# Kernel tuning notes

Hardware: AMD Instinct MI355X
Metric: run time of the kernel (lower is better)

The kernel has to match this reference:

```python
import jax, jax.numpy as jnp
import numpy as np

N_NODES = 100000


def _gcn_layer(x, src, dst, W, b, n_nodes):
    # x: [N, Cin]; src/dst already include self-loops
    h = x @ W  # [N, Cout]
    deg = jax.ops.segment_sum(jnp.ones_like(dst, dtype=h.dtype), dst,
                              num_segments=n_nodes)  # in-degree incl. self-loop
    dinv = jnp.where(deg > 0, deg ** -0.5, 0.0)
    norm = dinv[src] * dinv[dst]  # [E]
    msg = h[src] * norm[:, None]  # [E, Cout]
    out = jax.ops.segment_sum(msg, dst, num_segments=n_nodes)
    return out + b


def setup_inputs() -> dict:
    key = jax.random.key(0)
    k1, k2, k3, k4, k5, k6, k7 = jax.random.split(key, 7)
    E = 6400000
    x = jax.random.normal(k1, (N_NODES, 5), dtype=jnp.float32)
    edge_index = jax.random.randint(k2, (2, E), 0, N_NODES, dtype=jnp.int64)
    edge_f = jax.random.normal(k3, (E,), dtype=jnp.float32)
    edge_attr = jax.random.normal(k4, (E, 1), dtype=jnp.float32)
    # GCNConv params (glorot-ish scale)
    W1 = jax.random.normal(k5, (5, 8), dtype=jnp.float32) * (1.0 / np.sqrt(5))
    b1 = jnp.zeros((8,), dtype=jnp.float32)
    W2 = jax.random.normal(k6, (8, 5), dtype=jnp.float32) * (1.0 / np.sqrt(8))
    b2 = jnp.zeros((5,), dtype=jnp.float32)
    return {"x": x, "edge_index": edge_index, "edge_f": edge_f,
            "edge_attr": edge_attr, "W1": W1, "b1": b1, "W2": W2, "b2": b2}


def reference(x, edge_index, edge_f, edge_attr, W1, b1, W2, b2):
    n = x.shape[0]
    loops = jnp.arange(n, dtype=edge_index.dtype)
    src = jnp.concatenate([edge_index[0], loops])  # add self-loops (PyG default)
    dst = jnp.concatenate([edge_index[1], loops])
    h = _gcn_layer(x, src, dst, W1, b1, n)
    h = _gcn_layer(h, src, dst, W2, b2, n)
    return h
```

## Files before the change

kernel.cpp:

```cpp
#include <hip/hip_runtime.h>


#define TPB 256
#define VPB 256
#define B_BITS 8
#define MAXB 512
#define CAP 17408
#define NBLK_E 512
#define EPB 12500
#define SCT 512
#define DGT 512

typedef int int4e __attribute__((ext_vector_type(4)));
__device__ __forceinline__ int4e ntload4(const int* p) {
    return __builtin_nontemporal_load((const int4e*)p);
}
__device__ __forceinline__ int ntload(const int* p) {
    return __builtin_nontemporal_load(p);
}

__global__ void k_init(int B, int* __restrict__ bpos) {
    int b = blockIdx.x * blockDim.x + threadIdx.x;
    if (b < B) bpos[b] = b * CAP;
}

__global__ __launch_bounds__(SCT) void k_scat(const int* __restrict__ src,
        const int* __restrict__ dst, int E, int B,
        int* __restrict__ bpos, int* __restrict__ pairs) {
    __shared__ int sorted[EPB];
    __shared__ int hist[MAXB], scn[MAXB], cur[MAXB], gbase[MAXB];
    int t = threadIdx.x;
    for (int i = t; i < MAXB; i += SCT) hist[i] = 0;
    __syncthreads();
    int lo = blockIdx.x * EPB;
    int n = min(E - lo, EPB);
    int n4 = n & ~3;
    for (int i = t * 4; i < n4; i += SCT * 4) {
        int4e d4 = ntload4(dst + lo + i);
        atomicAdd(&hist[d4.x >> B_BITS], 1);
        atomicAdd(&hist[d4.y >> B_BITS], 1);
        atomicAdd(&hist[d4.z >> B_BITS], 1);
        atomicAdd(&hist[d4.w >> B_BITS], 1);
    }
    for (int i = n4 + t; i < n; i += SCT)
        atomicAdd(&hist[dst[lo + i] >> B_BITS], 1);
    __syncthreads();
    if (t < MAXB) scn[t] = hist[t];
    __syncthreads();
    for (int off = 1; off < MAXB; off <<= 1) {
        int v = (t >= off && t < MAXB) ? scn[t - off] : 0;
        __syncthreads();
        if (t < MAXB) scn[t] += v;
        __syncthreads();
    }
    if (t < MAXB) {
        int h = hist[t];
        cur[t] = scn[t] - h;
        gbase[t] = (t < B && h) ? atomicAdd(&bpos[t], h) : 0;
    }
    __syncthreads();
    for (int i = t * 4; i < n4; i += SCT * 4) {
        int4e d4 = ntload4(dst + lo + i);
        int4e s4 = ntload4(src + lo + i);
        int p;
        p = atomicAdd(&cur[d4.x >> B_BITS], 1); sorted[p] = (s4.x << B_BITS) | (d4.x & (VPB - 1));
        p = atomicAdd(&cur[d4.y >> B_BITS], 1); sorted[p] = (s4.y << B_BITS) | (d4.y & (VPB - 1));
        p = atomicAdd(&cur[d4.z >> B_BITS], 1); sorted[p] = (s4.z << B_BITS) | (d4.z & (VPB - 1));
        p = atomicAdd(&cur[d4.w >> B_BITS], 1); sorted[p] = (s4.w << B_BITS) | (d4.w & (VPB - 1));
    }
    for (int i = n4 + t; i < n; i += SCT) {
        int d = dst[lo + i], s = src[lo + i];
        int p = atomicAdd(&cur[d >> B_BITS], 1);
        sorted[p] = (s << B_BITS) | (d & (VPB - 1));
    }
    __syncthreads();
    int wave = t >> 6, lane = t & 63;
    for (int b2 = wave; b2 < B; b2 += (SCT >> 6)) {
        int h = hist[b2];
        int st = scn[b2] - h;
        int gb = gbase[b2];
        for (int j = lane; j < h; j += 64)
            pairs[gb + j] = sorted[st + j];
    }
}

__global__ __launch_bounds__(DGT) void k_degxs(const int* __restrict__ pairs,
        const int* __restrict__ bpos, int N,
        const float* __restrict__ x,
        unsigned int* __restrict__ jinfo, float* __restrict__ xs) {
    __shared__ int hist[VPB];
    __shared__ int scn[VPB];
    int t = threadIdx.x, b = blockIdx.x;
    if (t < VPB) hist[t] = 0;
    __syncthreads();
    int base = b * CAP;
    int n = bpos[b] - base, n4 = n & ~3;
    for (int i = t * 4; i < n4; i += DGT * 4) {
        int4e p = ntload4(pairs + base + i);
        atomicAdd(&hist[p.x & (VPB - 1)], 1);
        atomicAdd(&hist[p.y & (VPB - 1)], 1);
        atomicAdd(&hist[p.z & (VPB - 1)], 1);
        atomicAdd(&hist[p.w & (VPB - 1)], 1);
    }
    for (int i = n4 + t; i < n; i += DGT)
        atomicAdd(&hist[pairs[base + i] & (VPB - 1)], 1);
    __syncthreads();
    if (t < VPB) scn[t] = hist[t];
    __syncthreads();
    for (int off = 1; off < VPB; off <<= 1) {
        int v = (t >= off && t < VPB) ? scn[t - off] : 0;
        __syncthreads();
        if (t < VPB) scn[t] += v;
        __syncthreads();
    }
    int node = b * VPB + t;
    if (t < VPB && node < N) {
        int h = hist[t];
        int start = base + scn[t] - h;
        jinfo[node] = ((unsigned int)start << 9) | (unsigned int)h;
        float di = rsqrtf((float)(h + 1));
        const float* xp = x + (size_t)node * 5;
        float4 v4 = make_float4(xp[0] * di, xp[1] * di, xp[2] * di, xp[3] * di);
        *(float4*)(xs + (size_t)node * 8) = v4;
        xs[(size_t)node * 8 + 4] = xp[4] * di;
    }
}

__global__ __launch_bounds__(1024) void k_agg1(const int* __restrict__ pairs_,
        const int* __restrict__ bpos, const unsigned int* __restrict__ jinfo,
        const float* __restrict__ xs, const float* __restrict__ b1,
        const float* __restrict__ W1, const float* __restrict__ W2,
        float* __restrict__ h2s, int N) {
    __shared__ int csr[CAP];
    __shared__ int js[VPB], ct[VPB], cur[VPB];
    int* pairs = (int*)pairs_;
    int t = threadIdx.x, b = blockIdx.x;
    int base = b * CAP;
    if (t < VPB) {
        int node = b * VPB + t;
        int s = 0, c = 0;
        if (node < N) {
            unsigned int u = jinfo[node];
            s = (int)(u >> 9) - base;
            c = (int)(u & 511u);
        }
        js[t] = s; ct[t] = c; cur[t] = s;
    }
    __syncthreads();
    int n = bpos[b] - base, n4 = n & ~3;
    for (int i = t * 4; i < n4; i += 1024 * 4) {
        int4e p = ntload4(pairs + base + i);
        int q;
        q = atomicAdd(&cur[p.x & (VPB - 1)], 1); csr[q] = p.x >> B_BITS;
        q = atomicAdd(&cur[p.y & (VPB - 1)], 1); csr[q] = p.y >> B_BITS;
        q = atomicAdd(&cur[p.z & (VPB - 1)], 1); csr[q] = p.z >> B_BITS;
        q = atomicAdd(&cur[p.w & (VPB - 1)], 1); csr[q] = p.w >> B_BITS;
    }
    for (int i = n4 + t; i < n; i += 1024) {
        int p = pairs[base + i];
        int q = atomicAdd(&cur[p & (VPB - 1)], 1);
        csr[q] = p >> B_BITS;
    }
    __syncthreads();
    for (int i = t; i < n; i += 1024)
        __builtin_nontemporal_store(csr[i], pairs + base + i);
    int lane = t & 3, ln = t >> 2;
    int node = b * VPB + ln;
    if (node >= N) return;
    int s0 = js[ln], cn = ct[ln];
    float a0 = 0.f, a1 = 0.f, a2 = 0.f, a3 = 0.f, a4 = 0.f;
    int j = lane;
    for (; j + 4 < cn; j += 8) {
        int sA = csr[s0 + j];
        int sB = csr[s0 + j + 4];
        const float* pA = xs + (size_t)sA * 8;
        const float* pB = xs + (size_t)sB * 8;
        float4 xA = *(const float4*)pA; float eA = pA[4];
        float4 xB = *(const float4*)pB; float eB = pB[4];
        a0 += xA.x + xB.x; a1 += xA.y + xB.y; a2 += xA.z + xB.z;
        a3 += xA.w + xB.w; a4 += eA + eB;
    }
    if (j < cn) {
        int sA = csr[s0 + j];
        const float* pA = xs + (size_t)sA * 8;
        float4 xA = *(const float4*)pA;
        a0 += xA.x; a1 += xA.y; a2 += xA.z; a3 += xA.w; a4 += pA[4];
    }
#pragma unroll
    for (int d = 1; d < 4; d <<= 1) {
        a0 += __shfl_xor(a0, d); a1 += __shfl_xor(a1, d);
        a2 += __shfl_xor(a2, d); a3 += __shfl_xor(a3, d);
        a4 += __shfl_xor(a4, d);
    }
    const float* sp = xs + (size_t)node * 8;
    float4 sx = *(const float4*)sp;
    float tc[5];
    tc[0] = a0 + sx.x; tc[1] = a1 + sx.y; tc[2] = a2 + sx.z;
    tc[3] = a3 + sx.w; tc[4] = a4 + sp[4];
    float di = rsqrtf((float)(cn + 1));
    float o1[8];
#pragma unroll
    for (int jj = 0; jj < 8; ++jj) {
        float h = 0.f;
#pragma unroll
        for (int c = 0; c < 5; ++c) h += tc[c] * W1[c * 8 + jj];
        o1[jj] = h * di + b1[jj];
    }
    {
        float h = 0.f;
#pragma unroll
        for (int jj = 0; jj < 8; ++jj) h += o1[jj] * W2[jj * 5 + lane];
        h2s[(size_t)node * 8 + lane] = h * di;
        if (lane == 0) {
            float h4 = 0.f;
#pragma unroll
            for (int jj = 0; jj < 8; ++jj) h4 += o1[jj] * W2[jj * 5 + 4];
            h2s[(size_t)node * 8 + 4] = h4 * di;
        }
    }
}

__global__ __launch_bounds__(TPB) void k_agg2(const int* __restrict__ pairs,
        const unsigned int* __restrict__ jinfo, const float* __restrict__ h2s,
        const float* __restrict__ b2, float* __restrict__ out, int N) {
    int gid = blockIdx.x * blockDim.x + threadIdx.x;
    int node = gid >> 3, lane = gid & 7;
    if (node >= N) return;
    unsigned int u = jinfo[node];
    int jsa = (int)(u >> 9), cn = (int)(u & 511u);
    float a0 = 0.f, a1 = 0.f, a2 = 0.f, a3 = 0.f, a4 = 0.f;
    int j = lane;
    for (; j + 8 < cn; j += 16) {
        int sA = ntload(pairs + jsa + j);
        int sB = ntload(pairs + jsa + j + 8);
        const float* pA = h2s + (size_t)sA * 8;
        const float* pB = h2s + (size_t)sB * 8;
        float4 xA = *(const float4*)pA; float eA = pA[4];
        float4 xB = *(const float4*)pB; float eB = pB[4];
        a0 += xA.x + xB.x; a1 += xA.y + xB.y; a2 += xA.z + xB.z;
        a3 += xA.w + xB.w; a4 += eA + eB;
    }
    if (j < cn) {
        int sA = ntload(pairs + jsa + j);
        const float* pA = h2s + (size_t)sA * 8;
        float4 xA = *(const float4*)pA;
        a0 += xA.x; a1 += xA.y; a2 += xA.z; a3 += xA.w; a4 += pA[4];
    }
#pragma unroll
    for (int d = 1; d < 8; d <<= 1) {
        a0 += __shfl_xor(a0, d); a1 += __shfl_xor(a1, d);
        a2 += __shfl_xor(a2, d); a3 += __shfl_xor(a3, d);
        a4 += __shfl_xor(a4, d);
    }
    if (lane == 0) {
        float di = rsqrtf((float)(cn + 1));
        const float* sr = h2s + (size_t)node * 8;
        float* op = out + (size_t)node * 5;
        op[0] = (a0 + sr[0]) * di + b2[0];
        op[1] = (a1 + sr[1]) * di + b2[1];
        op[2] = (a2 + sr[2]) * di + b2[2];
        op[3] = (a3 + sr[3]) * di + b2[3];
        op[4] = (a4 + sr[4]) * di + b2[4];
    }
}

extern "C" void kernel_launch(void* const* d_in, const int* in_sizes, int n_in,
                              void* d_out, int out_size, void* d_ws, size_t ws_size,
                              hipStream_t stream) {
    const float* x   = (const float*)d_in[0];
    const int*  eidx = (const int*)d_in[1];
    const float* b1 = (const float*)d_in[5];
    const float* W1 = (const float*)d_in[4];
    const float* W2 = (const float*)d_in[6];
    const float* b2 = (const float*)d_in[7];
    float* out = (float*)d_out;

    const int N = in_sizes[0] / 5;
    const int E = in_sizes[1] / 2;
    const int* src = eidx;
    const int* dst = eidx + E;

    const int B = (N + VPB - 1) / VPB;

    int*   pairs = (int*)d_ws;
    float* xs    = (float*)(pairs + (size_t)B * CAP);
    float* h2s   = xs + (size_t)8 * N;
    unsigned int* jinfo = (unsigned int*)(h2s + (size_t)8 * N);
    int*   bpos  = (int*)(jinfo + N);

    const int g8N = (8 * N + TPB - 1) / TPB;

    k_init <<<(B + TPB - 1) / TPB, TPB, 0, stream>>>(B, bpos);
    k_scat <<<NBLK_E, SCT, 0, stream>>>(src, dst, E, B, bpos, pairs);
    k_degxs<<<B, DGT, 0, stream>>>(pairs, bpos, N, x, jinfo, xs);
    k_agg1 <<<B, 1024, 0, stream>>>(pairs, bpos, jinfo, xs, b1, W1, W2, h2s, N);
    k_agg2 <<<g8N, TPB, 0, stream>>>(pairs, jinfo, h2s, b2, out, N);
}
```

Before: 258.3 us.

## Store intermediate node features in fp16 and unroll gathers four-wide

Stores the normalized input features and the second-layer pre-aggregation features as 8-element fp16 vectors (16 bytes per node) instead of fp32 (32 bytes). Random gathers in both aggregation kernels then fetch a single 16-byte vector per neighbor, and the gather loops are unrolled to four neighbors per iteration. Accumulation stays in fp32. This is meant to halve gather traffic and improve cache hit rates, at the cost of fp16 rounding error in the intermediate features that could exceed tolerance.

```diff
diff --git a/kernel.cpp b/kernel.cpp
--- a/kernel.cpp
+++ b/kernel.cpp
@@ -1,4 +1,5 @@
 #include <hip/hip_runtime.h>
+#include <hip/hip_fp16.h>
 
 
 #define TPB 256
@@ -12,6 +13,8 @@
 #define DGT 512
 
 typedef int int4e __attribute__((ext_vector_type(4)));
+typedef _Float16 h8 __attribute__((ext_vector_type(8)));
+
 __device__ __forceinline__ int4e ntload4(const int* p) {
     return __builtin_nontemporal_load((const int4e*)p);
 }
@@ -87,7 +90,7 @@
 __global__ __launch_bounds__(DGT) void k_degxs(const int* __restrict__ pairs,
         const int* __restrict__ bpos, int N,
         const float* __restrict__ x,
-        unsigned int* __restrict__ jinfo, float* __restrict__ xs) {
+        unsigned int* __restrict__ jinfo, _Float16* __restrict__ xs) {
     __shared__ int hist[VPB];
     __shared__ int scn[VPB];
     int t = threadIdx.x, b = blockIdx.x;
@@ -120,17 +123,20 @@
         jinfo[node] = ((unsigned int)start << 9) | (unsigned int)h;
         float di = rsqrtf((float)(h + 1));
         const float* xp = x + (size_t)node * 5;
-        float4 v4 = make_float4(xp[0] * di, xp[1] * di, xp[2] * di, xp[3] * di);
-        *(float4*)(xs + (size_t)node * 8) = v4;
-        xs[(size_t)node * 8 + 4] = xp[4] * di;
+        h8 v;
+        v[0] = (_Float16)(xp[0] * di); v[1] = (_Float16)(xp[1] * di);
+        v[2] = (_Float16)(xp[2] * di); v[3] = (_Float16)(xp[3] * di);
+        v[4] = (_Float16)(xp[4] * di);
+        v[5] = (_Float16)0.f; v[6] = (_Float16)0.f; v[7] = (_Float16)0.f;
+        *(h8*)(xs + (size_t)node * 8) = v;
     }
 }
 
 __global__ __launch_bounds__(1024) void k_agg1(const int* __restrict__ pairs_,
         const int* __restrict__ bpos, const unsigned int* __restrict__ jinfo,
-        const float* __restrict__ xs, const float* __restrict__ b1,
+        const _Float16* __restrict__ xs, const float* __restrict__ b1,
         const float* __restrict__ W1, const float* __restrict__ W2,
-        float* __restrict__ h2s, int N) {
+        _Float16* __restrict__ h2s, int N) {
     __shared__ int csr[CAP];
     __shared__ int js[VPB], ct[VPB], cur[VPB];
     int* pairs = (int*)pairs_;
@@ -170,21 +176,26 @@
     int s0 = js[ln], cn = ct[ln];
     float a0 = 0.f, a1 = 0.f, a2 = 0.f, a3 = 0.f, a4 = 0.f;
     int j = lane;
-    for (; j + 4 < cn; j += 8) {
+    for (; j + 12 < cn; j += 16) {
         int sA = csr[s0 + j];
         int sB = csr[s0 + j + 4];
-        const float* pA = xs + (size_t)sA * 8;
-        const float* pB = xs + (size_t)sB * 8;
-        float4 xA = *(const float4*)pA; float eA = pA[4];
-        float4 xB = *(const float4*)pB; float eB = pB[4];
-        a0 += xA.x + xB.x; a1 += xA.y + xB.y; a2 += xA.z + xB.z;
-        a3 += xA.w + xB.w; a4 += eA + eB;
-    }
-    if (j < cn) {
+        int sC = csr[s0 + j + 8];
+        int sD = csr[s0 + j + 12];
+        h8 vA = *(const h8*)(xs + (size_t)sA * 8);
+        h8 vB = *(const h8*)(xs + (size_t)sB * 8);
+        h8 vC = *(const h8*)(xs + (size_t)sC * 8);
+        h8 vD = *(const h8*)(xs + (size_t)sD * 8);
+        a0 += (float)vA[0] + (float)vB[0] + (float)vC[0] + (float)vD[0];
+        a1 += (float)vA[1] + (float)vB[1] + (float)vC[1] + (float)vD[1];
+        a2 += (float)vA[2] + (float)vB[2] + (float)vC[2] + (float)vD[2];
+        a3 += (float)vA[3] + (float)vB[3] + (float)vC[3] + (float)vD[3];
+        a4 += (float)vA[4] + (float)vB[4] + (float)vC[4] + (float)vD[4];
+    }
+    for (; j < cn; j += 4) {
         int sA = csr[s0 + j];
-        const float* pA = xs + (size_t)sA * 8;
-        float4 xA = *(const float4*)pA;
-        a0 += xA.x; a1 += xA.y; a2 += xA.z; a3 += xA.w; a4 += pA[4];
+        h8 vA = *(const h8*)(xs + (size_t)sA * 8);
+        a0 += (float)vA[0]; a1 += (float)vA[1]; a2 += (float)vA[2];
+        a3 += (float)vA[3]; a4 += (float)vA[4];
     }
 #pragma unroll
     for (int d = 1; d < 4; d <<= 1) {
@@ -192,11 +203,11 @@
         a2 += __shfl_xor(a2, d); a3 += __shfl_xor(a3, d);
         a4 += __shfl_xor(a4, d);
     }
-    const float* sp = xs + (size_t)node * 8;
-    float4 sx = *(const float4*)sp;
+    h8 sv = *(const h8*)(xs + (size_t)node * 8);
     float tc[5];
-    tc[0] = a0 + sx.x; tc[1] = a1 + sx.y; tc[2] = a2 + sx.z;
-    tc[3] = a3 + sx.w; tc[4] = a4 + sp[4];
+    tc[0] = a0 + (float)sv[0]; tc[1] = a1 + (float)sv[1];
+    tc[2] = a2 + (float)sv[2]; tc[3] = a3 + (float)sv[3];
+    tc[4] = a4 + (float)sv[4];
     float di = rsqrtf((float)(cn + 1));
     float o1[8];
 #pragma unroll
@@ -206,22 +217,25 @@
         for (int c = 0; c < 5; ++c) h += tc[c] * W1[c * 8 + jj];
         o1[jj] = h * di + b1[jj];
     }
-    {
-        float h = 0.f;
-#pragma unroll
-        for (int jj = 0; jj < 8; ++jj) h += o1[jj] * W2[jj * 5 + lane];
-        h2s[(size_t)node * 8 + lane] = h * di;
-        if (lane == 0) {
-            float h4 = 0.f;
-#pragma unroll
-            for (int jj = 0; jj < 8; ++jj) h4 += o1[jj] * W2[jj * 5 + 4];
-            h2s[(size_t)node * 8 + 4] = h4 * di;
+    if (lane == 0) {
+        float hv[5];
+#pragma unroll
+        for (int k = 0; k < 5; ++k) {
+            float h = 0.f;
+#pragma unroll
+            for (int jj = 0; jj < 8; ++jj) h += o1[jj] * W2[jj * 5 + k];
+            hv[k] = h * di;
         }
+        h8 w;
+        w[0] = (_Float16)hv[0]; w[1] = (_Float16)hv[1]; w[2] = (_Float16)hv[2];
+        w[3] = (_Float16)hv[3]; w[4] = (_Float16)hv[4];
+        w[5] = (_Float16)0.f; w[6] = (_Float16)0.f; w[7] = (_Float16)0.f;
+        *(h8*)(h2s + (size_t)node * 8) = w;
     }
 }
 
 __global__ __launch_bounds__(TPB) void k_agg2(const int* __restrict__ pairs,
-        const unsigned int* __restrict__ jinfo, const float* __restrict__ h2s,
+        const unsigned int* __restrict__ jinfo, const _Float16* __restrict__ h2s,
         const float* __restrict__ b2, float* __restrict__ out, int N) {
     int gid = blockIdx.x * blockDim.x + threadIdx.x;
     int node = gid >> 3, lane = gid & 7;
@@ -230,21 +244,26 @@
     int jsa = (int)(u >> 9), cn = (int)(u & 511u);
     float a0 = 0.f, a1 = 0.f, a2 = 0.f, a3 = 0.f, a4 = 0.f;
     int j = lane;
-    for (; j + 8 < cn; j += 16) {
+    for (; j + 24 < cn; j += 32) {
         int sA = ntload(pairs + jsa + j);
         int sB = ntload(pairs + jsa + j + 8);
-        const float* pA = h2s + (size_t)sA * 8;
-        const float* pB = h2s + (size_t)sB * 8;
-        float4 xA = *(const float4*)pA; float eA = pA[4];
-        float4 xB = *(const float4*)pB; float eB = pB[4];
-        a0 += xA.x + xB.x; a1 += xA.y + xB.y; a2 += xA.z + xB.z;
-        a3 += xA.w + xB.w; a4 += eA + eB;
-    }
-    if (j < cn) {
+        int sC = ntload(pairs + jsa + j + 16);
+        int sD = ntload(pairs + jsa + j + 24);
+        h8 vA = *(const h8*)(h2s + (size_t)sA * 8);
+        h8 vB = *(const h8*)(h2s + (size_t)sB * 8);
+        h8 vC = *(const h8*)(h2s + (size_t)sC * 8);
+        h8 vD = *(const h8*)(h2s + (size_t)sD * 8);
+        a0 += (float)vA[0] + (float)vB[0] + (float)vC[0] + (float)vD[0];
+        a1 += (float)vA[1] + (float)vB[1] + (float)vC[1] + (float)vD[1];
+        a2 += (float)vA[2] + (float)vB[2] + (float)vC[2] + (float)vD[2];
+        a3 += (float)vA[3] + (float)vB[3] + (float)vC[3] + (float)vD[3];
+        a4 += (float)vA[4] + (float)vB[4] + (float)vC[4] + (float)vD[4];
+    }
+    for (; j < cn; j += 8) {
         int sA = ntload(pairs + jsa + j);
-        const float* pA = h2s + (size_t)sA * 8;
-        float4 xA = *(const float4*)pA;
-        a0 += xA.x; a1 += xA.y; a2 += xA.z; a3 += xA.w; a4 += pA[4];
+        h8 vA = *(const h8*)(h2s + (size_t)sA * 8);
+        a0 += (float)vA[0]; a1 += (float)vA[1]; a2 += (float)vA[2];
+        a3 += (float)vA[3]; a4 += (float)vA[4];
     }
 #pragma unroll
     for (int d = 1; d < 8; d <<= 1) {
@@ -254,13 +273,13 @@
     }
     if (lane == 0) {
         float di = rsqrtf((float)(cn + 1));
-        const float* sr = h2s + (size_t)node * 8;
+        h8 sv = *(const h8*)(h2s + (size_t)node * 8);
         float* op = out + (size_t)node * 5;
-        op[0] = (a0 + sr[0]) * di + b2[0];
-        op[1] = (a1 + sr[1]) * di + b2[1];
-        op[2] = (a2 + sr[2]) * di + b2[2];
-        op[3] = (a3 + sr[3]) * di + b2[3];
-        op[4] = (a4 + sr[4]) * di + b2[4];
+        op[0] = (a0 + (float)sv[0]) * di + b2[0];
+        op[1] = (a1 + (float)sv[1]) * di + b2[1];
+        op[2] = (a2 + (float)sv[2]) * di + b2[2];
+        op[3] = (a3 + (float)sv[3]) * di + b2[3];
+        op[4] = (a4 + (float)sv[4]) * di + b2[4];
     }
 }
 
@@ -269,8 +288,8 @@
                               hipStream_t stream) {
     const float* x   = (const float*)d_in[0];
     const int*  eidx = (const int*)d_in[1];
+    const float* W1 = (const float*)d_in[4];
     const float* b1 = (const float*)d_in[5];
-    const float* W1 = (const float*)d_in[4];
     const float* W2 = (const float*)d_in[6];
     const float* b2 = (const float*)d_in[7];
     float* out = (float*)d_out;
@@ -282,11 +301,11 @@
 
     const int B = (N + VPB - 1) / VPB;
 
-    int*   pairs = (int*)d_ws;
-    float* xs    = (float*)(pairs + (size_t)B * CAP);
-    float* h2s   = xs + (size_t)8 * N;
+    int*      pairs = (int*)d_ws;
+    _Float16* xs    = (_Float16*)(pairs + (size_t)B * CAP);
+    _Float16* h2s   = xs + (size_t)8 * N;
     unsigned int* jinfo = (unsigned int*)(h2s + (size_t)8 * N);
-    int*   bpos  = (int*)(jinfo + N);
+    int*      bpos  = (int*)(jinfo + N);
 
     const int g8N = (8 * N + TPB - 1) / TPB;
 
```

After: 243.8 us. 5.6% less time.
